# Kernel tuning notes

Hardware: AMD Instinct MI355X
Metric: run time of the kernel (lower is better)

## Reference

```python
import jax, jax.numpy as jnp
import numpy as np
import math

B, E, C = 1024, 512, 70722
M_COEF, H_COEF, SCALE, EPS = 0.4, 0.333, 64.0, 1e-3


def setup_inputs() -> dict:
    key = jax.random.key(0)
    k1, k2, k3, k4 = jax.random.split(key, 4)
    emb = jax.random.normal(k1, (B, E), dtype=jnp.float32)
    emb = emb / jnp.linalg.norm(emb, axis=1, keepdims=True)  # unit-norm face embeddings
    norms = jax.random.uniform(k2, (B, 1), dtype=jnp.float32) * 30.0 + 5.0  # feature norms ~[5,35]
    label = jax.random.randint(k3, (B,), 0, C)
    kernel = jax.random.uniform(k4, (E, C), dtype=jnp.float32, minval=-1.0, maxval=1.0)
    return {"embbedings": emb, "norms": norms, "label": label, "kernel": kernel}


def reference(embbedings, norms, label, kernel):
    # column-wise l2 norm of the class-weight kernel
    kernel_norm = kernel / jnp.linalg.norm(kernel, axis=0, keepdims=True)
    cosine = jnp.clip(embbedings @ kernel_norm, -1.0 + EPS, 1.0 - EPS)  # (B, C)

    # norms are detached in the original (safe_norms.clone().detach())
    safe_norms = jax.lax.stop_gradient(jnp.clip(norms, 1e-3, 100.0))  # (B, 1)
    # with t_alpha=1.0 the EMA buffers collapse to the current batch stats
    batch_mean = jnp.mean(safe_norms)
    batch_std = jnp.std(safe_norms, ddof=1)  # torch.std is unbiased
    margin_scaler = jnp.clip((safe_norms - batch_mean) / (batch_std + EPS) * H_COEF, -1.0, 1.0)[:, 0]  # (B,)

    g_angular = -M_COEF * margin_scaler          # additive angular margin, (B,)
    g_add = M_COEF + M_COEF * margin_scaler      # additive cosine margin, (B,)

    theta = jnp.arccos(cosine)                   # (B, C)
    rows = jnp.arange(B)
    theta = theta.at[rows, label].add(g_angular)  # one-hot scatter of angular margin
    theta = jnp.clip(theta, EPS, math.pi - EPS)
    cosine_m = jnp.cos(theta)
    cosine_m = cosine_m.at[rows, label].add(-g_add)  # one-hot scatter of cos margin
    return cosine_m * SCALE
```

## Files before the change

kernel.cpp:

```cpp
#include <hip/hip_runtime.h>
#include <hip/hip_bf16.h>

#define BDIM 1024
#define EDIM 512
#define CDIM 70722
#define NPAD 70784
#define SCALE 64.0f
#define EPS_C 1e-3f
#define M_COEF 0.4f
#define H_COEF 0.333f
#define PI_F 3.14159265358979323846f

using short8 = __attribute__((ext_vector_type(8))) short;
using f32x4  = __attribute__((ext_vector_type(4))) float;

__device__ __forceinline__ unsigned short f2bf(float f) {
    union { float f; unsigned int u; } x; x.f = f;
    unsigned int u = x.u;
    unsigned int r = (u + 0x7fffu + ((u >> 16) & 1u)) >> 16;
    return (unsigned short)r;
}

__global__ __launch_bounds__(256) void convert_transpose(
        const float* __restrict__ Kw, unsigned short* __restrict__ Bt,
        float* __restrict__ colsumsq) {
    __shared__ float tile[64][65];
    __shared__ float ssq[4][64];
    const int t  = threadIdx.x;
    const int n0 = blockIdx.x * 64;
    const int k0 = blockIdx.y * 64;
    const int nn = t & 63;
    const int kg = t >> 6;

    float s = 0.f;
    const int ng = n0 + nn;
#pragma unroll
    for (int rr = 0; rr < 16; ++rr) {
        const int kk = kg * 16 + rr;
        float v = (ng < CDIM) ? Kw[(size_t)(k0 + kk) * CDIM + ng] : 0.f;
        tile[kk][nn] = v;
        s += v * v;
    }
    ssq[kg][nn] = s;
    __syncthreads();

    if (t < 64) {
        float tot = ssq[0][t] + ssq[1][t] + ssq[2][t] + ssq[3][t];
        if (n0 + t < CDIM) atomicAdd(&colsumsq[n0 + t], tot);
    }

    const int k = t & 63;
    const int ngrp = t >> 6;
#pragma unroll
    for (int rr = 0; rr < 16; ++rr) {
        const int nl = ngrp * 16 + rr;
        float v = tile[k][nl];
        Bt[(size_t)(n0 + nl) * EDIM + k0 + k] = f2bf(v);
    }
}

__global__ __launch_bounds__(256) void inv_kernel(
        const float* __restrict__ colsumsq, float* __restrict__ inv_norm) {
    int n = blockIdx.x * 256 + threadIdx.x;
    if (n < NPAD) inv_norm[n] = (n < CDIM) ? (1.0f / sqrtf(colsumsq[n])) : 0.0f;
}

__global__ __launch_bounds__(256) void convert_A(
        const float* __restrict__ emb, unsigned short* __restrict__ Abf) {
    int i = (blockIdx.x * 256 + threadIdx.x) * 4;
    float4 v = *(const float4*)&emb[i];
    ushort4 o;
    o.x = f2bf(v.x); o.y = f2bf(v.y); o.z = f2bf(v.z); o.w = f2bf(v.w);
    *(ushort4*)&Abf[i] = o;
}

__global__ __launch_bounds__(256) void gemm_kernel(
        const unsigned short* __restrict__ A,
        const unsigned short* __restrict__ Bt,
        const float* __restrict__ inv_norm,
        float* __restrict__ out) {
    __shared__ unsigned short As[128 * 32];
    __shared__ unsigned short Bs[128 * 32];

    const int tid  = threadIdx.x;
    const int w    = tid >> 6;
    const int lane = tid & 63;
    const int wm   = w >> 1;
    const int wn   = w & 1;
    const int m0   = blockIdx.y * 128;
    const int n0   = blockIdx.x * 128;

    f32x4 acc[4][4] = {};

    const int lrow = lane & 15;
    const int koff = (lane >> 4) * 8;

    for (int kt = 0; kt < EDIM / 32; ++kt) {
        const int k0 = kt * 32;
        __syncthreads();
#pragma unroll
        for (int j = 0; j < 2; ++j) {
            const int chunk = j * 256 + tid;
            const int r = chunk >> 2;
            const int c = (chunk & 3) << 3;
            const unsigned short* ga = A  + (size_t)(m0 + r) * EDIM + (k0 + c);
            const unsigned short* gb = Bt + (size_t)(n0 + r) * EDIM + (k0 + c);
            char* la = (char*)As + (j * 4 + w) * 1024;
            char* lb = (char*)Bs + (j * 4 + w) * 1024;
            __builtin_amdgcn_global_load_lds(
                (const __attribute__((address_space(1))) void*)ga,
                (__attribute__((address_space(3))) void*)la, 16, 0, 0);
            __builtin_amdgcn_global_load_lds(
                (const __attribute__((address_space(1))) void*)gb,
                (__attribute__((address_space(3))) void*)lb, 16, 0, 0);
        }
        asm volatile("s_waitcnt vmcnt(0)" ::: "memory");
        __syncthreads();

        short8 af[4], bf[4];
#pragma unroll
        for (int f = 0; f < 4; ++f) {
            af[f] = *(const short8*)&As[(wm * 64 + f * 16 + lrow) * 32 + koff];
            bf[f] = *(const short8*)&Bs[(wn * 64 + f * 16 + lrow) * 32 + koff];
        }
#pragma unroll
        for (int i = 0; i < 4; ++i)
#pragma unroll
            for (int jj = 0; jj < 4; ++jj)
                acc[i][jj] = __builtin_amdgcn_mfma_f32_16x16x32_bf16(
                    af[i], bf[jj], acc[i][jj], 0, 0, 0);
    }

    const int colBase = n0 + wn * 64 + (lane & 15);
    const int rowBase = m0 + wm * 64 + (lane >> 4) * 4;
#pragma unroll
    for (int jj = 0; jj < 4; ++jj) {
        const int cg = colBase + jj * 16;
        if (cg < CDIM) {
            const float invn = inv_norm[cg];
#pragma unroll
            for (int i = 0; i < 4; ++i) {
#pragma unroll
                for (int r = 0; r < 4; ++r) {
                    const int rg = rowBase + i * 16 + r;
                    float v = acc[i][jj][r] * invn;
                    v = fminf(fmaxf(v, -1.0f + EPS_C), 1.0f - EPS_C);
                    out[(size_t)rg * CDIM + cg] = v * SCALE;
                }
            }
        }
    }
}

__global__ __launch_bounds__(1024) void fixup_kernel(
        const float* __restrict__ norms, const int* __restrict__ label,
        float* __restrict__ out) {
    __shared__ float red[1024];
    const int t = threadIdx.x;
    const float x = fminf(fmaxf(norms[t], 1e-3f), 100.0f);

    red[t] = x;
    __syncthreads();
#pragma unroll
    for (int s = 512; s > 0; s >>= 1) {
        if (t < s) red[t] += red[t + s];
        __syncthreads();
    }
    const float mean = red[0] * (1.0f / 1024.0f);
    __syncthreads();

    const float d = x - mean;
    red[t] = d * d;
    __syncthreads();
#pragma unroll
    for (int s = 512; s > 0; s >>= 1) {
        if (t < s) red[t] += red[t + s];
        __syncthreads();
    }
    const float stdv = sqrtf(red[0] * (1.0f / 1023.0f));

    float ms = (x - mean) / (stdv + EPS_C) * H_COEF;
    ms = fminf(fmaxf(ms, -1.0f), 1.0f);
    const float g_ang = -M_COEF * ms;
    const float g_add = M_COEF + M_COEF * ms;

    const size_t idx = (size_t)t * CDIM + label[t];
    const float c = out[idx] * (1.0f / SCALE);
    float theta = acosf(c) + g_ang;
    theta = fminf(fmaxf(theta, EPS_C), PI_F - EPS_C);
    out[idx] = (cosf(theta) - g_add) * SCALE;
}

extern "C" void kernel_launch(void* const* d_in, const int* in_sizes, int n_in,
                              void* d_out, int out_size, void* d_ws, size_t ws_size,
                              hipStream_t stream) {
    const float* emb   = (const float*)d_in[0];
    const float* norms = (const float*)d_in[1];
    const int*   label = (const int*)d_in[2];
    const float* Kw    = (const float*)d_in[3];
    float* out = (float*)d_out;

    char* ws = (char*)d_ws;
    float* colsumsq          = (float*)(ws + 0);
    float* inv_norm          = (float*)(ws + 283136);
    unsigned short* Abf      = (unsigned short*)(ws + 566272);
    unsigned short* Bt       = (unsigned short*)(ws + 1614848);

    hipMemsetAsync(colsumsq, 0, NPAD * sizeof(float), stream);

    convert_transpose<<<dim3(NPAD / 64, EDIM / 64), 256, 0, stream>>>(Kw, Bt, colsumsq);
    inv_kernel<<<dim3((NPAD + 255) / 256), 256, 0, stream>>>(colsumsq, inv_norm);
    convert_A<<<dim3(BDIM * EDIM / (256 * 4)), 256, 0, stream>>>(emb, Abf);
    gemm_kernel<<<dim3(NPAD / 128, BDIM / 128), 256, 0, stream>>>(Abf, Bt, inv_norm, out);
    fixup_kernel<<<1, 1024, 0, stream>>>(norms, label, out);
}
```

Before: 572.9 us.

## Fuse kernel conversion, transpose and column norms into the GEMM

Removes the separate convert_transpose, inv_kernel and memset passes. The GEMM now reads the fp32 class-weight matrix directly, transposes and converts it to bf16 through shared memory each K step, and accumulates the column sum of squares in-block to compute the inverse norms. It also adds an XOR swizzle to the LDS layouts to reduce bank conflicts and a grouped block ordering that places the 8 M-blocks of each N column together for L2 reuse. In exchange, each block converts B itself, so the fp32 kernel is read 8 times (once per M-block, hopefully from L2) and extra VALU and LDS work lands inside the GEMM loop.

```diff
diff --git a/kernel.cpp b/kernel.cpp
--- a/kernel.cpp
+++ b/kernel.cpp
@@ -4,7 +4,6 @@
 #define BDIM 1024
 #define EDIM 512
 #define CDIM 70722
-#define NPAD 70784
 #define SCALE 64.0f
 #define EPS_C 1e-3f
 #define M_COEF 0.4f
@@ -19,50 +18,6 @@
     unsigned int u = x.u;
     unsigned int r = (u + 0x7fffu + ((u >> 16) & 1u)) >> 16;
     return (unsigned short)r;
-}
-
-__global__ __launch_bounds__(256) void convert_transpose(
-        const float* __restrict__ Kw, unsigned short* __restrict__ Bt,
-        float* __restrict__ colsumsq) {
-    __shared__ float tile[64][65];
-    __shared__ float ssq[4][64];
-    const int t  = threadIdx.x;
-    const int n0 = blockIdx.x * 64;
-    const int k0 = blockIdx.y * 64;
-    const int nn = t & 63;
-    const int kg = t >> 6;
-
-    float s = 0.f;
-    const int ng = n0 + nn;
-#pragma unroll
-    for (int rr = 0; rr < 16; ++rr) {
-        const int kk = kg * 16 + rr;
-        float v = (ng < CDIM) ? Kw[(size_t)(k0 + kk) * CDIM + ng] : 0.f;
-        tile[kk][nn] = v;
-        s += v * v;
-    }
-    ssq[kg][nn] = s;
-    __syncthreads();
-
-    if (t < 64) {
-        float tot = ssq[0][t] + ssq[1][t] + ssq[2][t] + ssq[3][t];
-        if (n0 + t < CDIM) atomicAdd(&colsumsq[n0 + t], tot);
-    }
-
-    const int k = t & 63;
-    const int ngrp = t >> 6;
-#pragma unroll
-    for (int rr = 0; rr < 16; ++rr) {
-        const int nl = ngrp * 16 + rr;
-        float v = tile[k][nl];
-        Bt[(size_t)(n0 + nl) * EDIM + k0 + k] = f2bf(v);
-    }
-}
-
-__global__ __launch_bounds__(256) void inv_kernel(
-        const float* __restrict__ colsumsq, float* __restrict__ inv_norm) {
-    int n = blockIdx.x * 256 + threadIdx.x;
-    if (n < NPAD) inv_norm[n] = (n < CDIM) ? (1.0f / sqrtf(colsumsq[n])) : 0.0f;
 }
 
 __global__ __launch_bounds__(256) void convert_A(
@@ -74,54 +29,110 @@
     *(ushort4*)&Abf[i] = o;
 }
 
-__global__ __launch_bounds__(256) void gemm_kernel(
+__global__ __launch_bounds__(256) void gemm_fused(
         const unsigned short* __restrict__ A,
-        const unsigned short* __restrict__ Bt,
-        const float* __restrict__ inv_norm,
+        const float* __restrict__ Kw,
         float* __restrict__ out) {
     __shared__ unsigned short As[128 * 32];
     __shared__ unsigned short Bs[128 * 32];
+    __shared__ float Tf[32 * 132];
+
+    const int bid = blockIdx.x;
+    int m_blk, n_blk;
+    if (bid < 4416) {
+        const int x = bid & 7;
+        const int j = bid >> 3;
+        n_blk = ((j >> 3) << 3) + x;
+        m_blk = j & 7;
+    } else {
+        n_blk = 552;
+        m_blk = bid - 4416;
+    }
+    const int m0 = m_blk << 7;
+    const int n0 = n_blk << 7;
 
     const int tid  = threadIdx.x;
     const int w    = tid >> 6;
     const int lane = tid & 63;
     const int wm   = w >> 1;
     const int wn   = w & 1;
-    const int m0   = blockIdx.y * 128;
-    const int n0   = blockIdx.x * 128;
+    const int lrow = lane & 15;
+    const int khf  = lane >> 4;
+    const int gsw  = (lrow >> 1) & 3;
 
     f32x4 acc[4][4] = {};
-
-    const int lrow = lane & 15;
-    const int koff = (lane >> 4) * 8;
-
-    for (int kt = 0; kt < EDIM / 32; ++kt) {
-        const int k0 = kt * 32;
-        __syncthreads();
+    float ssq0 = 0.f, ssq1 = 0.f, ssq2 = 0.f, ssq3 = 0.f;
+
+    const int bl_c = (tid & 31) << 2;
+    const int bl_r = tid >> 5;
+    const float* bptr = Kw + (size_t)bl_r * CDIM + n0 + bl_c;
+    const bool edge = (n_blk == 552);
+    const int  crem = CDIM - n0;
+
+    for (int kt = 0; kt < 16; ++kt) {
+        const int k0 = kt << 5;
+        __syncthreads();
+
+        float4 bv[4];
+        const float* bp = bptr + (size_t)k0 * CDIM;
+#pragma unroll
+        for (int p = 0; p < 4; ++p) {
+            const float* rp = bp + (size_t)(p << 3) * CDIM;
+            if (!edge) {
+                bv[p] = *(const float4*)rp;
+            } else {
+                float* e = (float*)&bv[p];
+                e[0] = (bl_c + 0 < crem) ? rp[0] : 0.f;
+                e[1] = (bl_c + 1 < crem) ? rp[1] : 0.f;
+                e[2] = (bl_c + 2 < crem) ? rp[2] : 0.f;
+                e[3] = (bl_c + 3 < crem) ? rp[3] : 0.f;
+            }
+        }
+
 #pragma unroll
         for (int j = 0; j < 2; ++j) {
-            const int chunk = j * 256 + tid;
-            const int r = chunk >> 2;
-            const int c = (chunk & 3) << 3;
-            const unsigned short* ga = A  + (size_t)(m0 + r) * EDIM + (k0 + c);
-            const unsigned short* gb = Bt + (size_t)(n0 + r) * EDIM + (k0 + c);
-            char* la = (char*)As + (j * 4 + w) * 1024;
-            char* lb = (char*)Bs + (j * 4 + w) * 1024;
+            const int sigma = (((j << 2) + w) << 6) + lane;
+            const int r  = sigma >> 2;
+            const int kh = (sigma & 3) ^ ((r >> 1) & 3);
+            const unsigned short* ga = A + (size_t)(m0 + r) * EDIM + k0 + (kh << 3);
             __builtin_amdgcn_global_load_lds(
                 (const __attribute__((address_space(1))) void*)ga,
-                (__attribute__((address_space(3))) void*)la, 16, 0, 0);
-            __builtin_amdgcn_global_load_lds(
-                (const __attribute__((address_space(1))) void*)gb,
-                (__attribute__((address_space(3))) void*)lb, 16, 0, 0);
-        }
+                (__attribute__((address_space(3))) void*)((char*)As + (((j << 2) + w) << 10)),
+                16, 0, 0);
+        }
+
+#pragma unroll
+        for (int p = 0; p < 4; ++p) {
+            *(float4*)&Tf[(((p << 3) + bl_r) * 132) + bl_c] = bv[p];
+            const float* e = (const float*)&bv[p];
+            ssq0 += e[0] * e[0]; ssq1 += e[1] * e[1];
+            ssq2 += e[2] * e[2]; ssq3 += e[3] * e[3];
+        }
+        __syncthreads();
+
+        const int bn = tid >> 1;
+        const int kb = (tid & 1) << 4;
+        short8 t0, t1;
+#pragma unroll
+        for (int jj = 0; jj < 8; ++jj) t0[jj] = (short)f2bf(Tf[(kb + jj) * 132 + bn]);
+#pragma unroll
+        for (int jj = 0; jj < 8; ++jj) t1[jj] = (short)f2bf(Tf[(kb + 8 + jj) * 132 + bn]);
+        const int gswn = (bn >> 1) & 3;
+        const int kh0  = (((tid & 1) << 1) + 0) ^ gswn;
+        const int kh1  = (((tid & 1) << 1) + 1) ^ gswn;
+        *(short8*)((char*)Bs + (((bn << 2) + kh0) << 4)) = t0;
+        *(short8*)((char*)Bs + (((bn << 2) + kh1) << 4)) = t1;
+
         asm volatile("s_waitcnt vmcnt(0)" ::: "memory");
         __syncthreads();
 
         short8 af[4], bf[4];
 #pragma unroll
         for (int f = 0; f < 4; ++f) {
-            af[f] = *(const short8*)&As[(wm * 64 + f * 16 + lrow) * 32 + koff];
-            bf[f] = *(const short8*)&Bs[(wn * 64 + f * 16 + lrow) * 32 + koff];
+            const int ar = (wm << 6) + (f << 4) + lrow;
+            af[f] = *(const short8*)((const char*)As + (((ar << 2) + (khf ^ gsw)) << 4));
+            const int br = (wn << 6) + (f << 4) + lrow;
+            bf[f] = *(const short8*)((const char*)Bs + (((br << 2) + (khf ^ gsw)) << 4));
         }
 #pragma unroll
         for (int i = 0; i < 4; ++i)
@@ -131,18 +142,33 @@
                     af[i], bf[jj], acc[i][jj], 0, 0, 0);
     }
 
-    const int colBase = n0 + wn * 64 + (lane & 15);
-    const int rowBase = m0 + wm * 64 + (lane >> 4) * 4;
+    __syncthreads();
+    float* sred = Tf;
+    const int sbase = (bl_r << 7) + bl_c;
+    sred[sbase + 0] = ssq0; sred[sbase + 1] = ssq1;
+    sred[sbase + 2] = ssq2; sred[sbase + 3] = ssq3;
+    __syncthreads();
+    if (tid < 128) {
+        float s = 0.f;
+#pragma unroll
+        for (int r = 0; r < 8; ++r) s += sred[(r << 7) + tid];
+        sred[1024 + tid] = rsqrtf(s);
+    }
+    __syncthreads();
+
+    const int colLoc  = (wn << 6) + lrow;
+    const int rowBase = m0 + (wm << 6) + (khf << 2);
 #pragma unroll
     for (int jj = 0; jj < 4; ++jj) {
-        const int cg = colBase + jj * 16;
+        const int cl = colLoc + (jj << 4);
+        const int cg = n0 + cl;
         if (cg < CDIM) {
-            const float invn = inv_norm[cg];
+            const float invn = sred[1024 + cl];
 #pragma unroll
             for (int i = 0; i < 4; ++i) {
 #pragma unroll
                 for (int r = 0; r < 4; ++r) {
-                    const int rg = rowBase + i * 16 + r;
+                    const int rg = rowBase + (i << 4) + r;
                     float v = acc[i][jj][r] * invn;
                     v = fminf(fmaxf(v, -1.0f + EPS_C), 1.0f - EPS_C);
                     out[(size_t)rg * CDIM + cg] = v * SCALE;
@@ -200,17 +226,9 @@
     const float* Kw    = (const float*)d_in[3];
     float* out = (float*)d_out;
 
-    char* ws = (char*)d_ws;
-    float* colsumsq          = (float*)(ws + 0);
-    float* inv_norm          = (float*)(ws + 283136);
-    unsigned short* Abf      = (unsigned short*)(ws + 566272);
-    unsigned short* Bt       = (unsigned short*)(ws + 1614848);
-
-    hipMemsetAsync(colsumsq, 0, NPAD * sizeof(float), stream);
-
-    convert_transpose<<<dim3(NPAD / 64, EDIM / 64), 256, 0, stream>>>(Kw, Bt, colsumsq);
-    inv_kernel<<<dim3((NPAD + 255) / 256), 256, 0, stream>>>(colsumsq, inv_norm);
+    unsigned short* Abf = (unsigned short*)d_ws;
+
     convert_A<<<dim3(BDIM * EDIM / (256 * 4)), 256, 0, stream>>>(emb, Abf);
-    gemm_kernel<<<dim3(NPAD / 128, BDIM / 128), 256, 0, stream>>>(Abf, Bt, inv_norm, out);
+    gemm_fused<<<dim3(553 * 8), 256, 0, stream>>>(Abf, Kw, out);
     fixup_kernel<<<1, 1024, 0, stream>>>(norms, label, out);
 }
```

Measured after the change: 638.0 us. +11.4%, slower.
